# Kernel tuning notes

Measured on AMD Instinct MI355X. Metric: run time of the kernel, lower is better.

The kernel has to match this reference:

```python
import jax, jax.numpy as jnp
import numpy as np

EMBED = 64
SQ = (2, 2)
SHUF = 2
EXPAN = 2
SQ_CH = EMBED // SQ[0]            # 32
SHUF_SP = SQ_CH * SHUF * SHUF     # 128
SQ_SP = SHUF_SP // SQ[1]          # 64
NH = SQ_CH * EXPAN                # 64 heads (same for both attentions)
DN = ('NCHW', 'OIHW', 'NCHW')


def _l2norm(x, axis):
    return x / jnp.maximum(jnp.linalg.norm(x, axis=axis, keepdims=True), 1e-12)


def _qkv_depthwise(x, w, b):
    # grouped 1x1 conv with groups == C: each input channel c maps to 3*EXPAN outputs
    # x: [B,C,H,W], w/b: [C, 3*EXPAN] -> [B, 3*EXPAN, C, H, W]
    y = x[:, :, None] * w[None, :, :, None, None] + b[None, :, :, None, None]
    return jnp.swapaxes(y, 1, 2)


def _group_fuse(o, wf, bf):
    # grouped 1x1 conv groups==C: o [B,C,EXPAN,H,W], wf [C,EXPAN], bf [C]
    return jnp.einsum('bcehw,ce->bchw', o, wf) + bf[None, :, None, None]


def _attention(x, wqkv, bqkv, t, wf, bf, spatial):
    B, C, H, W = x.shape
    qkv = _qkv_depthwise(x, wqkv, bqkv)            # [B, 3*EXPAN, C, H, W]
    d = EXPAN * C // NH                            # head dim over channels
    hw = H * W
    heads = lambda a: a.reshape(B, NH, d, hw)
    q = heads(qkv[:, :EXPAN])
    k = heads(qkv[:, EXPAN:2 * EXPAN])
    v = heads(qkv[:, 2 * EXPAN:])
    if spatial:
        q, k = _l2norm(q, -2), _l2norm(k, -2)
        attn = jax.nn.softmax(jnp.einsum('bhdn,bhdm->bhnm', q, k) * t, axis=-1)
        o = jnp.einsum('bhnm,bhdm->bhdn', attn, v)
    else:
        q, k = _l2norm(q, -1), _l2norm(k, -1)
        attn = jax.nn.softmax(jnp.einsum('bhdn,bhen->bhde', q, k) * t, axis=-1)
        o = jnp.einsum('bhde,bhen->bhdn', attn, v)
    # [B,NH,d,HW] -> [B,EXPAN,C,H,W] -> [B,C,EXPAN,H,W]
    o = o.reshape(B, EXPAN, C, H, W).transpose(0, 2, 1, 3, 4)
    return _group_fuse(o, wf, bf)


def setup_inputs() -> dict:
    key = jax.random.key(0)
    ks = jax.random.split(key, 20)
    s = 0.02
    inp = {
        'x': jax.random.normal(ks[0], (2, EMBED, 64, 64), jnp.float32),
        'w_sq1': jax.random.normal(ks[1], (SQ_CH, EMBED), jnp.float32) * s,
        'b_sq1': jax.random.normal(ks[2], (SQ_CH,), jnp.float32) * s,
        'w_sq2': jax.random.normal(ks[3], (SQ_SP, 1, SHUF, SHUF), jnp.float32) * s,
        'b_sq2': jax.random.normal(ks[4], (SQ_SP,), jnp.float32) * s,
        'ca_wqkv': jax.random.normal(ks[5], (SQ_SP, 3 * EXPAN), jnp.float32) * s,
        'ca_bqkv': jax.random.normal(ks[6], (SQ_SP, 3 * EXPAN), jnp.float32) * s,
        'ca_t': jnp.ones((1, NH, 1, 1), jnp.float32),
        'ca_wf': jax.random.normal(ks[7], (SQ_SP, EXPAN), jnp.float32) * s,
        'ca_bf': jax.random.normal(ks[8], (SQ_SP,), jnp.float32) * s,
        'sa_wqkv': jax.random.normal(ks[9], (SQ_SP, 3 * EXPAN), jnp.float32) * s,
        'sa_bqkv': jax.random.normal(ks[10], (SQ_SP, 3 * EXPAN), jnp.float32) * s,
        'sa_t': jnp.ones((1, NH, 1, 1), jnp.float32),
        'sa_wf': jax.random.normal(ks[11], (SQ_SP, EXPAN), jnp.float32) * s,
        'sa_bf': jax.random.normal(ks[12], (SQ_SP,), jnp.float32) * s,
        'w_un1': jax.random.normal(ks[13], (SHUF_SP, SQ_SP // SQ_CH, 1, 1), jnp.float32) * s,
        'b_un1': jax.random.normal(ks[14], (SHUF_SP,), jnp.float32) * s,
        'w_un2': jax.random.normal(ks[15], (EMBED, SQ_CH), jnp.float32) * s,
        'b_un2': jax.random.normal(ks[16], (EMBED,), jnp.float32) * s,
    }
    return inp


def reference(x, w_sq1, b_sq1, w_sq2, b_sq2,
              ca_wqkv, ca_bqkv, ca_t, ca_wf, ca_bf,
              sa_wqkv, sa_bqkv, sa_t, sa_wf, sa_bf,
              w_un1, b_un1, w_un2, b_un2):
    # ch_sp_squeeze: 1x1 conv then grouped shuffle-stride conv
    y = jnp.einsum('bchw,oc->bohw', x, w_sq1) + b_sq1[None, :, None, None]
    y = jax.lax.conv_general_dilated(y, w_sq2, (SHUF, SHUF), 'VALID',
                                     feature_group_count=SQ_CH,
                                     dimension_numbers=DN) + b_sq2[None, :, None, None]
    group_num, each_group = SQ_CH, SQ_SP // SQ_CH
    idx = np.array([i + j * group_num for i in range(group_num) for j in range(each_group)])
    y = y[:, idx]
    y = _attention(y, ca_wqkv, ca_bqkv, ca_t, ca_wf, ca_bf, spatial=False)
    nidx = np.array([i + j * each_group for i in range(each_group) for j in range(group_num)])
    y = y[:, nidx]
    y = _attention(y, sa_wqkv, sa_bqkv, sa_t, sa_wf, sa_bf, spatial=True)
    # sp_ch_unsqueeze: grouped 1x1 conv, pixel shuffle, 1x1 conv
    y = jax.lax.conv_general_dilated(y, w_un1, (1, 1), 'VALID',
                                     feature_group_count=SQ_CH,
                                     dimension_numbers=DN) + b_un1[None, :, None, None]
    B, Cc, h, w = y.shape
    r = SHUF
    y = y.reshape(B, Cc // (r * r), r, r, h, w).transpose(0, 1, 4, 2, 5, 3)
    y = y.reshape(B, Cc // (r * r), h * r, w * r)
    y = jnp.einsum('bchw,oc->bohw', y, w_un2) + b_un2[None, :, None, None]
    return y
```

## Files before the change

kernel.cpp:

```cpp
#include <hip/hip_runtime.h>
#include <math.h>

#define NR 6

typedef float v2f __attribute__((ext_vector_type(2)));

__device__ __forceinline__ v2f vfma2(v2f a, v2f b, v2f c) {
#if defined(__has_builtin)
#if __has_builtin(__builtin_elementwise_fma)
    return __builtin_elementwise_fma(a, b, c);
#else
    v2f r; r.x = fmaf(a.x, b.x, c.x); r.y = fmaf(a.y, b.y, c.y); return r;
#endif
#else
    v2f r; r.x = fmaf(a.x, b.x, c.x); r.y = fmaf(a.y, b.y, c.y); return r;
#endif
}

__device__ __forceinline__ void bessel_J(float t, float* J) {
    float h = 0.5f * t, q = h * h;
    float hp = 1.f, rf = 1.f;
#pragma unroll
    for (int r = 0; r <= NR; ++r) {
        if (r > 0) { hp *= h; rf *= (1.f / r); }
        float term = hp * rf, sum = term;
#pragma unroll
        for (int k = 1; k <= 12; ++k) {
            term *= q * (1.f / (k * (r + k)));
            sum += term;
        }
        J[r] = (r ? 2.f : 1.f) * sum;
    }
}

__global__ __launch_bounds__(256) void k_front(const float* __restrict__ x,
        const float* __restrict__ w1x1, const float* __restrict__ b1x1,
        const float* __restrict__ wdw,  const float* __restrict__ bdw,
        float* __restrict__ y3) {
    __shared__ float lxs[64 * 128];
    __shared__ float lwt[8][64];
    int tid = threadIdx.x;
    int q   = blockIdx.x & 3;
    int i32 = (blockIdx.x >> 2) & 31;
    int b   = blockIdx.x >> 7;

    const float4* x4 = (const float4*)x;
#pragma unroll
    for (int i = 0; i < 8; ++i) {
        int f4 = tid + i * 256;
        int c  = f4 >> 5, cw = f4 & 31;
        ((float4*)lxs)[f4] = x4[(b * 64 + c) * 1024 + i32 * 32 + cw];
    }
    for (int idx = tid; idx < 512; idx += 256) {
        int gi = idx >> 6, c = idx & 63;
        int g = 4 * q + (gi & 3) + ((gi & 4) << 2);
        lwt[gi][c] = w1x1[g * 64 + c];
    }
    __syncthreads();

    int gidx = tid >> 5, col = tid & 31;
    int g = 4 * q + (gidx & 3) + ((gidx & 4) << 2);
    v2f acc0 = {0.f, 0.f}, acc1 = {0.f, 0.f};
    const v2f* lx2 = (const v2f*)lxs;
#pragma unroll 4
    for (int c = 0; c < 64; ++c) {
        float wv = lwt[gidx][c];
        v2f w2 = {wv, wv};
        acc0 = vfma2(w2, lx2[c * 64 + col], acc0);
        acc1 = vfma2(w2, lx2[c * 64 + 32 + col], acc1);
    }
    float bs = b1x1[g];
    float a00 = acc0.x + bs, a01 = acc0.y + bs;
    float a10 = acc1.x + bs, a11 = acc1.y + bs;
#pragma unroll
    for (int s = 0; s < 2; ++s) {
        int oc = 2 * g + s;
        int k  = 2 * (oc & 31) + (oc >> 5);
        float4 wd = ((const float4*)wdw)[oc];
        float v = bdw[oc];
        v = fmaf(wd.x, a00, v); v = fmaf(wd.y, a01, v);
        v = fmaf(wd.z, a10, v); v = fmaf(wd.w, a11, v);
        y3[(b * 64 + k) * 1024 + i32 * 32 + col] = v;
    }
}

__device__ __forceinline__ void ca_coeffs(int p, int d,
        float s00, float s01, float s11, float m0, float m1,
        const float* __restrict__ wqkv, const float* __restrict__ bqkv,
        const float* __restrict__ t,    const float* __restrict__ wf,
        const float* __restrict__ bf,   float& A, float& B, float& C) {
    const float N = 1024.f;
    int c0 = 2 * p, c1 = 2 * p + 1;
    int c  = 2 * p + d;
    float Aa = 0.f, Bb = 0.f, Cc = 0.f;
#pragma unroll
    for (int e = 0; e < 2; ++e) {
        float wq0 = wqkv[c0 * 6 + e],     wq1 = wqkv[c1 * 6 + e];
        float bq0 = bqkv[c0 * 6 + e],     bq1 = bqkv[c1 * 6 + e];
        float wk0 = wqkv[c0 * 6 + 2 + e], wk1 = wqkv[c1 * 6 + 2 + e];
        float bk0 = bqkv[c0 * 6 + 2 + e], bk1 = bqkv[c1 * 6 + 2 + e];
        float wv0 = wqkv[c0 * 6 + 4 + e], wv1 = wqkv[c1 * 6 + 4 + e];
        float bv0 = bqkv[c0 * 6 + 4 + e], bv1 = bqkv[c1 * 6 + 4 + e];
        float te  = t[e * 32 + p];
        float sqq = (d == 0) ? (wq0 * wq0 * s00 + 2.f * wq0 * bq0 * m0 + N * bq0 * bq0)
                             : (wq1 * wq1 * s11 + 2.f * wq1 * bq1 * m1 + N * bq1 * bq1);
        float kk0 = wk0 * wk0 * s00 + 2.f * wk0 * bk0 * m0 + N * bk0 * bk0;
        float kk1 = wk1 * wk1 * s11 + 2.f * wk1 * bk1 * m1 + N * bk1 * bk1;
        float inq  = 1.f / fmaxf(sqrtf(fmaxf(sqq, 0.f)), 1e-12f);
        float ink0 = 1.f / fmaxf(sqrtf(fmaxf(kk0, 0.f)), 1e-12f);
        float ink1 = 1.f / fmaxf(sqrtf(fmaxf(kk1, 0.f)), 1e-12f);
        float qk0 = (d == 0) ? (wq0 * wk0 * s00 + wq0 * bk0 * m0 + bq0 * wk0 * m0 + N * bq0 * bk0)
                             : (wq1 * wk0 * s01 + wq1 * bk0 * m1 + bq1 * wk0 * m0 + N * bq1 * bk0);
        float qk1 = (d == 0) ? (wq0 * wk1 * s01 + wq0 * bk1 * m0 + bq0 * wk1 * m1 + N * bq0 * bk1)
                             : (wq1 * wk1 * s11 + wq1 * bk1 * m1 + bq1 * wk1 * m1 + N * bq1 * bk1);
        float L0 = qk0 * inq * ink0 * te, L1 = qk1 * inq * ink1 * te;
        float mx = fmaxf(L0, L1);
        float e0 = expf(L0 - mx), e1 = expf(L1 - mx);
        float iv = 1.f / (e0 + e1);
        float p0 = e0 * iv, p1 = e1 * iv;
        float f = wf[c * 2 + e];
        Aa += f * p0 * wv0;
        Bb += f * p1 * wv1;
        Cc += f * (p0 * bv0 + p1 * bv1);
    }
    A = Aa; B = Bb; C = Cc + bf[c];
}

__global__ __launch_bounds__(256) void k_attn(const float* __restrict__ y3,
        const float* __restrict__ ca_wqkv, const float* __restrict__ ca_bqkv,
        const float* __restrict__ ca_t,    const float* __restrict__ ca_wf,
        const float* __restrict__ ca_bf,
        const float* __restrict__ wqkv, const float* __restrict__ bqkv,
        const float* __restrict__ t,    const float* __restrict__ wf,
        const float* __restrict__ bfuse, const float* __restrict__ w1,
        const float* __restrict__ b1,   float* __restrict__ y8) {
    __shared__ float ly[4][1024];
    __shared__ float redg[10][4];
    __shared__ float redm[4][39];
    __shared__ float momf[2][39];
    int tid = threadIdx.x;
    int chunk = blockIdx.x & 3;
    int j = (blockIdx.x >> 2) & 31;
    int b = blockIdx.x >> 7;
    int jp = j & 15;
    int dsel = j >> 4;
    int c0 = 2 * j, c1 = 2 * j + 1;

    const float* base = y3 + (b * 64 + 4 * jp) * 1024;
    float sA00 = 0, sA01 = 0, sA11 = 0, mA0 = 0, mA1 = 0;
    float sB00 = 0, sB01 = 0, sB11 = 0, mB0 = 0, mB1 = 0;
#pragma unroll
    for (int r = 0; r < 4; ++r) {
        int n = tid + r * 256;
        float a0 = base[n], a1 = base[1024 + n];
        float a2 = base[2048 + n], a3 = base[3072 + n];
        ly[0][n] = a0; ly[1][n] = a1; ly[2][n] = a2; ly[3][n] = a3;
        sA00 = fmaf(a0, a0, sA00); sA01 = fmaf(a0, a1, sA01); sA11 = fmaf(a1, a1, sA11);
        mA0 += a0; mA1 += a1;
        sB00 = fmaf(a2, a2, sB00); sB01 = fmaf(a2, a3, sB01); sB11 = fmaf(a3, a3, sB11);
        mB0 += a2; mB1 += a3;
    }
#pragma unroll
    for (int off = 1; off < 64; off <<= 1) {
        sA00 += __shfl_xor(sA00, off, 64); sA01 += __shfl_xor(sA01, off, 64);
        sA11 += __shfl_xor(sA11, off, 64); mA0 += __shfl_xor(mA0, off, 64);
        mA1  += __shfl_xor(mA1,  off, 64);
        sB00 += __shfl_xor(sB00, off, 64); sB01 += __shfl_xor(sB01, off, 64);
        sB11 += __shfl_xor(sB11, off, 64); mB0 += __shfl_xor(mB0, off, 64);
        mB1  += __shfl_xor(mB1,  off, 64);
    }
    int wid = tid >> 6;
    if ((tid & 63) == 0) {
        redg[0][wid] = sA00; redg[1][wid] = sA01; redg[2][wid] = sA11;
        redg[3][wid] = mA0;  redg[4][wid] = mA1;
        redg[5][wid] = sB00; redg[6][wid] = sB01; redg[7][wid] = sB11;
        redg[8][wid] = mB0;  redg[9][wid] = mB1;
    }
    __syncthreads();
    sA00 = redg[0][0] + redg[0][1] + redg[0][2] + redg[0][3];
    sA01 = redg[1][0] + redg[1][1] + redg[1][2] + redg[1][3];
    sA11 = redg[2][0] + redg[2][1] + redg[2][2] + redg[2][3];
    mA0  = redg[3][0] + redg[3][1] + redg[3][2] + redg[3][3];
    mA1  = redg[4][0] + redg[4][1] + redg[4][2] + redg[4][3];
    sB00 = redg[5][0] + redg[5][1] + redg[5][2] + redg[5][3];
    sB01 = redg[6][0] + redg[6][1] + redg[6][2] + redg[6][3];
    sB11 = redg[7][0] + redg[7][1] + redg[7][2] + redg[7][3];
    mB0  = redg[8][0] + redg[8][1] + redg[8][2] + redg[8][3];
    mB1  = redg[9][0] + redg[9][1] + redg[9][2] + redg[9][3];

    float Aa, Ba, Ca, Ab, Bb, Cb;
    ca_coeffs(2 * jp,     dsel, sA00, sA01, sA11, mA0, mA1,
              ca_wqkv, ca_bqkv, ca_t, ca_wf, ca_bf, Aa, Ba, Ca);
    ca_coeffs(2 * jp + 1, dsel, sB00, sB01, sB11, mB0, mB1,
              ca_wqkv, ca_bqkv, ca_t, ca_wf, ca_bf, Ab, Bb, Cb);

    int e2 = tid >> 7, l = tid & 127;
    float wk0 = wqkv[c0 * 6 + 2 + e2], wk1 = wqkv[c1 * 6 + 2 + e2];
    float bk0 = bqkv[c0 * 6 + 2 + e2], bk1 = bqkv[c1 * 6 + 2 + e2];
    float wv0 = wqkv[c0 * 6 + 4 + e2], wv1 = wqkv[c1 * 6 + 4 + e2];
    float bv0 = bqkv[c0 * 6 + 4 + e2], bv1 = bqkv[c1 * 6 + 4 + e2];
    float mom[39];
#pragma unroll
    for (int i = 0; i < 39; ++i) mom[i] = 0.f;
#pragma unroll
    for (int kk = 0; kk < 8; ++kk) {
        int m = l + (kk << 7);
        float xa = fmaf(Aa, ly[0][m], fmaf(Ba, ly[1][m], Ca));
        float xb = fmaf(Ab, ly[2][m], fmaf(Bb, ly[3][m], Cb));
        float k0 = fmaf(wk0, xa, bk0), k1 = fmaf(wk1, xb, bk1);
        float inv = 1.f / fmaxf(sqrtf(k0 * k0 + k1 * k1), 1e-12f);
        float cp = k0 * inv, sp = k1 * inv;
        float v0 = fmaf(wv0, xa, bv0), v1 = fmaf(wv1, xb, bv1);
        mom[0] += 1.f; mom[1] += v0; mom[2] += v1;
        float c_m1 = 1.f, s_m1 = 0.f, c_r = cp, s_r = sp;
        float twoc = 2.f * cp;
#pragma unroll
        for (int r = 1; r <= NR; ++r) {
            int bi = 3 + (r - 1) * 6;
            mom[bi + 0] += c_r;
            mom[bi + 1] = fmaf(c_r, v0, mom[bi + 1]);
            mom[bi + 2] = fmaf(c_r, v1, mom[bi + 2]);
            mom[bi + 3] += s_r;
            mom[bi + 4] = fmaf(s_r, v0, mom[bi + 4]);
            mom[bi + 5] = fmaf(s_r, v1, mom[bi + 5]);
            float cn = fmaf(twoc, c_r, -c_m1);
            float sn = fmaf(twoc, s_r, -s_m1);
            c_m1 = c_r; s_m1 = s_r; c_r = cn; s_r = sn;
        }
    }
#pragma unroll
    for (int i = 0; i < 39; ++i) {
        float v = mom[i];
        v += __shfl_xor(v, 1, 64);  v += __shfl_xor(v, 2, 64);
        v += __shfl_xor(v, 4, 64);  v += __shfl_xor(v, 8, 64);
        v += __shfl_xor(v, 16, 64); v += __shfl_xor(v, 32, 64);
        mom[i] = v;
    }
    if ((tid & 63) == 0) {
#pragma unroll
        for (int i = 0; i < 39; ++i) redm[wid][i] = mom[i];
    }
    __syncthreads();
    if (tid < 78) {
        int e = (tid >= 39) ? 1 : 0;
        int i = tid - 39 * e;
        int r = (i < 3) ? 0 : ((i - 3) / 6 + 1);
        float J[NR + 1];
        bessel_J(t[e * 32 + j], J);
        momf[e][i] = (redm[2 * e][i] + redm[2 * e + 1][i]) * J[r];
    }
    __syncthreads();

    int n = (chunk << 8) + tid;
    float xan = fmaf(Aa, ly[0][n], fmaf(Ba, ly[1][n], Ca));
    float xbn = fmaf(Ab, ly[2][n], fmaf(Bb, ly[3][n], Cb));
    float oo[2][2];
#pragma unroll
    for (int e = 0; e < 2; ++e) {
        float wq0 = wqkv[c0 * 6 + e], wq1 = wqkv[c1 * 6 + e];
        float bq0 = bqkv[c0 * 6 + e], bq1 = bqkv[c1 * 6 + e];
        float q0 = fmaf(wq0, xan, bq0), q1 = fmaf(wq1, xbn, bq1);
        float qi = 1.f / fmaxf(sqrtf(q0 * q0 + q1 * q1), 1e-12f);
        float a = q0 * qi, bq = q1 * qi;
        const float* M = momf[e];
        float den = M[0], o0 = M[1], o1 = M[2];
        float c_m1 = 1.f, s_m1 = 0.f, c_r = a, s_r = bq;
        float twoc = 2.f * a;
#pragma unroll
        for (int r = 1; r <= NR; ++r) {
            int bi = 3 + (r - 1) * 6;
            den = fmaf(c_r, M[bi + 0], den);
            o0  = fmaf(c_r, M[bi + 1], o0);
            o1  = fmaf(c_r, M[bi + 2], o1);
            den = fmaf(s_r, M[bi + 3], den);
            o0  = fmaf(s_r, M[bi + 4], o0);
            o1  = fmaf(s_r, M[bi + 5], o1);
            float cn = fmaf(twoc, c_r, -c_m1);
            float sn = fmaf(twoc, s_r, -s_m1);
            c_m1 = c_r; s_m1 = s_r; c_r = cn; s_r = sn;
        }
        float rr = 1.f / den;
        oo[e][0] = o0 * rr;
        oo[e][1] = o1 * rr;
    }
    float t0 = fmaf(wf[c0 * 2], oo[0][0], fmaf(wf[c0 * 2 + 1], oo[1][0], bfuse[c0]));
    float t1 = fmaf(wf[c1 * 2], oo[0][1], fmaf(wf[c1 * 2 + 1], oo[1][1], bfuse[c1]));
    int i32 = n >> 5, j32 = n & 31;
    float* dst = y8 + (b * 32 + j) * 4096 + (i32 * 2) * 64 + j32 * 2;
    float z0 = fmaf(w1[(4 * j + 0) * 2], t0, fmaf(w1[(4 * j + 0) * 2 + 1], t1, b1[4 * j + 0]));
    float z1 = fmaf(w1[(4 * j + 1) * 2], t0, fmaf(w1[(4 * j + 1) * 2 + 1], t1, b1[4 * j + 1]));
    float z2 = fmaf(w1[(4 * j + 2) * 2], t0, fmaf(w1[(4 * j + 2) * 2 + 1], t1, b1[4 * j + 2]));
    float z3 = fmaf(w1[(4 * j + 3) * 2], t0, fmaf(w1[(4 * j + 3) * 2 + 1], t1, b1[4 * j + 3]));
    *(float2*)(dst)      = make_float2(z0, z1);
    *(float2*)(dst + 64) = make_float2(z2, z3);
}

__global__ __launch_bounds__(256) void k_conv_un2(const float* __restrict__ y8,
        const float* __restrict__ w, const float* __restrict__ bias,
        float* __restrict__ out) {
    __shared__ float lx[32 * 64];
    __shared__ float lw[64 * 32];
    int tid = threadIdx.x;
    int gp0 = blockIdx.x * 64;
    int b = gp0 >> 12;
    int p0 = gp0 & 4095;
    for (int idx = tid; idx < 32 * 64; idx += 256) {
        int g = idx >> 6, pp = idx & 63;
        lx[idx] = y8[(b * 32 + g) * 4096 + p0 + pp];
    }
    for (int idx = tid; idx < 64 * 32; idx += 256) lw[idx] = w[idx];
    __syncthreads();
    int px = tid & 63, og = tid >> 6;
    float acc[16];
#pragma unroll
    for (int k = 0; k < 16; ++k) acc[k] = 0.f;
    for (int g = 0; g < 32; ++g) {
        float xv = lx[g * 64 + px];
#pragma unroll
        for (int k = 0; k < 16; ++k)
            acc[k] = fmaf(lw[(og * 16 + k) * 32 + g], xv, acc[k]);
    }
#pragma unroll
    for (int k = 0; k < 16; ++k) {
        int o = og * 16 + k;
        out[(b * 64 + o) * 4096 + p0 + px] = acc[k] + bias[o];
    }
}

extern "C" void kernel_launch(void* const* d_in, const int* in_sizes, int n_in,
                              void* d_out, int out_size, void* d_ws, size_t ws_size,
                              hipStream_t stream) {
    (void)in_sizes; (void)n_in; (void)out_size; (void)ws_size;
    const float* x       = (const float*)d_in[0];
    const float* w_sq1   = (const float*)d_in[1];
    const float* b_sq1   = (const float*)d_in[2];
    const float* w_sq2   = (const float*)d_in[3];
    const float* b_sq2   = (const float*)d_in[4];
    const float* ca_wqkv = (const float*)d_in[5];
    const float* ca_bqkv = (const float*)d_in[6];
    const float* ca_t    = (const float*)d_in[7];
    const float* ca_wf   = (const float*)d_in[8];
    const float* ca_bf   = (const float*)d_in[9];
    const float* sa_wqkv = (const float*)d_in[10];
    const float* sa_bqkv = (const float*)d_in[11];
    const float* sa_t    = (const float*)d_in[12];
    const float* sa_wf   = (const float*)d_in[13];
    const float* sa_bf   = (const float*)d_in[14];
    const float* w_un1   = (const float*)d_in[15];
    const float* b_un1   = (const float*)d_in[16];
    const float* w_un2   = (const float*)d_in[17];
    const float* b_un2   = (const float*)d_in[18];
    float* out = (float*)d_out;
    float* ws  = (float*)d_ws;
    float* y3 = ws;
    float* y8 = ws + 131072;

    k_front<<<256, 256, 0, stream>>>(x, w_sq1, b_sq1, w_sq2, b_sq2, y3);
    k_attn <<<256, 256, 0, stream>>>(y3, ca_wqkv, ca_bqkv, ca_t, ca_wf, ca_bf,
                                     sa_wqkv, sa_bqkv, sa_t, sa_wf, sa_bf,
                                     w_un1, b_un1, y8);
    k_conv_un2<<<128, 256, 0, stream>>>(y8, w_un2, b_un2, out);
}
```

Baseline: 110.5 us.

## Fuse three kernels into one persistent kernel with software grid barriers

Merges the front conv, attention and final 1x1 conv kernels into a single launch of 256 blocks, separated by atomic-counter grid barriers, with shared memory unioned across phases. The last phase is re-tiled to 32 pixels per block so it also uses 256 blocks. The goal is to remove inter-kernel launch gaps and tail drain. In exchange it adds a memset and spin-wait barriers, and it depends on all 256 blocks being co-resident to avoid deadlock.

```diff
diff --git a/kernel.cpp b/kernel.cpp
--- a/kernel.cpp
+++ b/kernel.cpp
@@ -30,57 +30,6 @@
             sum += term;
         }
         J[r] = (r ? 2.f : 1.f) * sum;
-    }
-}
-
-__global__ __launch_bounds__(256) void k_front(const float* __restrict__ x,
-        const float* __restrict__ w1x1, const float* __restrict__ b1x1,
-        const float* __restrict__ wdw,  const float* __restrict__ bdw,
-        float* __restrict__ y3) {
-    __shared__ float lxs[64 * 128];
-    __shared__ float lwt[8][64];
-    int tid = threadIdx.x;
-    int q   = blockIdx.x & 3;
-    int i32 = (blockIdx.x >> 2) & 31;
-    int b   = blockIdx.x >> 7;
-
-    const float4* x4 = (const float4*)x;
-#pragma unroll
-    for (int i = 0; i < 8; ++i) {
-        int f4 = tid + i * 256;
-        int c  = f4 >> 5, cw = f4 & 31;
-        ((float4*)lxs)[f4] = x4[(b * 64 + c) * 1024 + i32 * 32 + cw];
-    }
-    for (int idx = tid; idx < 512; idx += 256) {
-        int gi = idx >> 6, c = idx & 63;
-        int g = 4 * q + (gi & 3) + ((gi & 4) << 2);
-        lwt[gi][c] = w1x1[g * 64 + c];
-    }
-    __syncthreads();
-
-    int gidx = tid >> 5, col = tid & 31;
-    int g = 4 * q + (gidx & 3) + ((gidx & 4) << 2);
-    v2f acc0 = {0.f, 0.f}, acc1 = {0.f, 0.f};
-    const v2f* lx2 = (const v2f*)lxs;
-#pragma unroll 4
-    for (int c = 0; c < 64; ++c) {
-        float wv = lwt[gidx][c];
-        v2f w2 = {wv, wv};
-        acc0 = vfma2(w2, lx2[c * 64 + col], acc0);
-        acc1 = vfma2(w2, lx2[c * 64 + 32 + col], acc1);
-    }
-    float bs = b1x1[g];
-    float a00 = acc0.x + bs, a01 = acc0.y + bs;
-    float a10 = acc1.x + bs, a11 = acc1.y + bs;
-#pragma unroll
-    for (int s = 0; s < 2; ++s) {
-        int oc = 2 * g + s;
-        int k  = 2 * (oc & 31) + (oc >> 5);
-        float4 wd = ((const float4*)wdw)[oc];
-        float v = bdw[oc];
-        v = fmaf(wd.x, a00, v); v = fmaf(wd.y, a01, v);
-        v = fmaf(wd.z, a10, v); v = fmaf(wd.w, a11, v);
-        y3[(b * 64 + k) * 1024 + i32 * 32 + col] = v;
     }
 }
 
@@ -126,204 +75,268 @@
     A = Aa; B = Bb; C = Cc + bf[c];
 }
 
-__global__ __launch_bounds__(256) void k_attn(const float* __restrict__ y3,
+struct SmemF { float lxs[64 * 128]; float lwt[8][64]; };
+struct SmemA { float ly[4][1024]; float redg[10][4]; float redm[4][39]; float momf[2][39]; };
+struct SmemC { float lx[32 * 32]; float lw[64 * 32]; };
+union SmemU { SmemF f; SmemA a; SmemC c; };
+
+__device__ __forceinline__ void grid_bar(unsigned* cnt, unsigned target) {
+    __syncthreads();
+    if (threadIdx.x == 0) {
+        __hip_atomic_fetch_add(cnt, 1u, __ATOMIC_ACQ_REL, __HIP_MEMORY_SCOPE_AGENT);
+        while (__hip_atomic_load(cnt, __ATOMIC_ACQUIRE, __HIP_MEMORY_SCOPE_AGENT) < target)
+            __builtin_amdgcn_s_sleep(1);
+    }
+    __syncthreads();
+}
+
+__global__ __launch_bounds__(256) void k_fused(
+        const float* __restrict__ x,
+        const float* __restrict__ w1x1, const float* __restrict__ b1x1,
+        const float* __restrict__ wdw,  const float* __restrict__ bdw,
         const float* __restrict__ ca_wqkv, const float* __restrict__ ca_bqkv,
         const float* __restrict__ ca_t,    const float* __restrict__ ca_wf,
         const float* __restrict__ ca_bf,
         const float* __restrict__ wqkv, const float* __restrict__ bqkv,
         const float* __restrict__ t,    const float* __restrict__ wf,
         const float* __restrict__ bfuse, const float* __restrict__ w1,
-        const float* __restrict__ b1,   float* __restrict__ y8) {
-    __shared__ float ly[4][1024];
-    __shared__ float redg[10][4];
-    __shared__ float redm[4][39];
-    __shared__ float momf[2][39];
+        const float* __restrict__ b1,
+        const float* __restrict__ w2,   const float* __restrict__ b2,
+        float* __restrict__ y3, float* __restrict__ y8,
+        float* __restrict__ out, unsigned* __restrict__ bar) {
+    __shared__ __align__(16) SmemU sm;
     int tid = threadIdx.x;
-    int chunk = blockIdx.x & 3;
-    int j = (blockIdx.x >> 2) & 31;
-    int b = blockIdx.x >> 7;
-    int jp = j & 15;
-    int dsel = j >> 4;
-    int c0 = 2 * j, c1 = 2 * j + 1;
-
-    const float* base = y3 + (b * 64 + 4 * jp) * 1024;
-    float sA00 = 0, sA01 = 0, sA11 = 0, mA0 = 0, mA1 = 0;
-    float sB00 = 0, sB01 = 0, sB11 = 0, mB0 = 0, mB1 = 0;
-#pragma unroll
-    for (int r = 0; r < 4; ++r) {
-        int n = tid + r * 256;
-        float a0 = base[n], a1 = base[1024 + n];
-        float a2 = base[2048 + n], a3 = base[3072 + n];
-        ly[0][n] = a0; ly[1][n] = a1; ly[2][n] = a2; ly[3][n] = a3;
-        sA00 = fmaf(a0, a0, sA00); sA01 = fmaf(a0, a1, sA01); sA11 = fmaf(a1, a1, sA11);
-        mA0 += a0; mA1 += a1;
-        sB00 = fmaf(a2, a2, sB00); sB01 = fmaf(a2, a3, sB01); sB11 = fmaf(a3, a3, sB11);
-        mB0 += a2; mB1 += a3;
-    }
-#pragma unroll
-    for (int off = 1; off < 64; off <<= 1) {
-        sA00 += __shfl_xor(sA00, off, 64); sA01 += __shfl_xor(sA01, off, 64);
-        sA11 += __shfl_xor(sA11, off, 64); mA0 += __shfl_xor(mA0, off, 64);
-        mA1  += __shfl_xor(mA1,  off, 64);
-        sB00 += __shfl_xor(sB00, off, 64); sB01 += __shfl_xor(sB01, off, 64);
-        sB11 += __shfl_xor(sB11, off, 64); mB0 += __shfl_xor(mB0, off, 64);
-        mB1  += __shfl_xor(mB1,  off, 64);
-    }
-    int wid = tid >> 6;
-    if ((tid & 63) == 0) {
-        redg[0][wid] = sA00; redg[1][wid] = sA01; redg[2][wid] = sA11;
-        redg[3][wid] = mA0;  redg[4][wid] = mA1;
-        redg[5][wid] = sB00; redg[6][wid] = sB01; redg[7][wid] = sB11;
-        redg[8][wid] = mB0;  redg[9][wid] = mB1;
-    }
-    __syncthreads();
-    sA00 = redg[0][0] + redg[0][1] + redg[0][2] + redg[0][3];
-    sA01 = redg[1][0] + redg[1][1] + redg[1][2] + redg[1][3];
-    sA11 = redg[2][0] + redg[2][1] + redg[2][2] + redg[2][3];
-    mA0  = redg[3][0] + redg[3][1] + redg[3][2] + redg[3][3];
-    mA1  = redg[4][0] + redg[4][1] + redg[4][2] + redg[4][3];
-    sB00 = redg[5][0] + redg[5][1] + redg[5][2] + redg[5][3];
-    sB01 = redg[6][0] + redg[6][1] + redg[6][2] + redg[6][3];
-    sB11 = redg[7][0] + redg[7][1] + redg[7][2] + redg[7][3];
-    mB0  = redg[8][0] + redg[8][1] + redg[8][2] + redg[8][3];
-    mB1  = redg[9][0] + redg[9][1] + redg[9][2] + redg[9][3];
-
-    float Aa, Ba, Ca, Ab, Bb, Cb;
-    ca_coeffs(2 * jp,     dsel, sA00, sA01, sA11, mA0, mA1,
-              ca_wqkv, ca_bqkv, ca_t, ca_wf, ca_bf, Aa, Ba, Ca);
-    ca_coeffs(2 * jp + 1, dsel, sB00, sB01, sB11, mB0, mB1,
-              ca_wqkv, ca_bqkv, ca_t, ca_wf, ca_bf, Ab, Bb, Cb);
-
-    int e2 = tid >> 7, l = tid & 127;
-    float wk0 = wqkv[c0 * 6 + 2 + e2], wk1 = wqkv[c1 * 6 + 2 + e2];
-    float bk0 = bqkv[c0 * 6 + 2 + e2], bk1 = bqkv[c1 * 6 + 2 + e2];
-    float wv0 = wqkv[c0 * 6 + 4 + e2], wv1 = wqkv[c1 * 6 + 4 + e2];
-    float bv0 = bqkv[c0 * 6 + 4 + e2], bv1 = bqkv[c1 * 6 + 4 + e2];
-    float mom[39];
-#pragma unroll
-    for (int i = 0; i < 39; ++i) mom[i] = 0.f;
-#pragma unroll
-    for (int kk = 0; kk < 8; ++kk) {
-        int m = l + (kk << 7);
-        float xa = fmaf(Aa, ly[0][m], fmaf(Ba, ly[1][m], Ca));
-        float xb = fmaf(Ab, ly[2][m], fmaf(Bb, ly[3][m], Cb));
-        float k0 = fmaf(wk0, xa, bk0), k1 = fmaf(wk1, xb, bk1);
-        float inv = 1.f / fmaxf(sqrtf(k0 * k0 + k1 * k1), 1e-12f);
-        float cp = k0 * inv, sp = k1 * inv;
-        float v0 = fmaf(wv0, xa, bv0), v1 = fmaf(wv1, xb, bv1);
-        mom[0] += 1.f; mom[1] += v0; mom[2] += v1;
-        float c_m1 = 1.f, s_m1 = 0.f, c_r = cp, s_r = sp;
-        float twoc = 2.f * cp;
-#pragma unroll
-        for (int r = 1; r <= NR; ++r) {
-            int bi = 3 + (r - 1) * 6;
-            mom[bi + 0] += c_r;
-            mom[bi + 1] = fmaf(c_r, v0, mom[bi + 1]);
-            mom[bi + 2] = fmaf(c_r, v1, mom[bi + 2]);
-            mom[bi + 3] += s_r;
-            mom[bi + 4] = fmaf(s_r, v0, mom[bi + 4]);
-            mom[bi + 5] = fmaf(s_r, v1, mom[bi + 5]);
-            float cn = fmaf(twoc, c_r, -c_m1);
-            float sn = fmaf(twoc, s_r, -s_m1);
-            c_m1 = c_r; s_m1 = s_r; c_r = cn; s_r = sn;
-        }
-    }
-#pragma unroll
-    for (int i = 0; i < 39; ++i) {
-        float v = mom[i];
-        v += __shfl_xor(v, 1, 64);  v += __shfl_xor(v, 2, 64);
-        v += __shfl_xor(v, 4, 64);  v += __shfl_xor(v, 8, 64);
-        v += __shfl_xor(v, 16, 64); v += __shfl_xor(v, 32, 64);
-        mom[i] = v;
-    }
-    if ((tid & 63) == 0) {
-#pragma unroll
-        for (int i = 0; i < 39; ++i) redm[wid][i] = mom[i];
-    }
-    __syncthreads();
-    if (tid < 78) {
-        int e = (tid >= 39) ? 1 : 0;
-        int i = tid - 39 * e;
-        int r = (i < 3) ? 0 : ((i - 3) / 6 + 1);
-        float J[NR + 1];
-        bessel_J(t[e * 32 + j], J);
-        momf[e][i] = (redm[2 * e][i] + redm[2 * e + 1][i]) * J[r];
-    }
-    __syncthreads();
-
-    int n = (chunk << 8) + tid;
-    float xan = fmaf(Aa, ly[0][n], fmaf(Ba, ly[1][n], Ca));
-    float xbn = fmaf(Ab, ly[2][n], fmaf(Bb, ly[3][n], Cb));
-    float oo[2][2];
-#pragma unroll
-    for (int e = 0; e < 2; ++e) {
-        float wq0 = wqkv[c0 * 6 + e], wq1 = wqkv[c1 * 6 + e];
-        float bq0 = bqkv[c0 * 6 + e], bq1 = bqkv[c1 * 6 + e];
-        float q0 = fmaf(wq0, xan, bq0), q1 = fmaf(wq1, xbn, bq1);
-        float qi = 1.f / fmaxf(sqrtf(q0 * q0 + q1 * q1), 1e-12f);
-        float a = q0 * qi, bq = q1 * qi;
-        const float* M = momf[e];
-        float den = M[0], o0 = M[1], o1 = M[2];
-        float c_m1 = 1.f, s_m1 = 0.f, c_r = a, s_r = bq;
-        float twoc = 2.f * a;
-#pragma unroll
-        for (int r = 1; r <= NR; ++r) {
-            int bi = 3 + (r - 1) * 6;
-            den = fmaf(c_r, M[bi + 0], den);
-            o0  = fmaf(c_r, M[bi + 1], o0);
-            o1  = fmaf(c_r, M[bi + 2], o1);
-            den = fmaf(s_r, M[bi + 3], den);
-            o0  = fmaf(s_r, M[bi + 4], o0);
-            o1  = fmaf(s_r, M[bi + 5], o1);
-            float cn = fmaf(twoc, c_r, -c_m1);
-            float sn = fmaf(twoc, s_r, -s_m1);
-            c_m1 = c_r; s_m1 = s_r; c_r = cn; s_r = sn;
-        }
-        float rr = 1.f / den;
-        oo[e][0] = o0 * rr;
-        oo[e][1] = o1 * rr;
-    }
-    float t0 = fmaf(wf[c0 * 2], oo[0][0], fmaf(wf[c0 * 2 + 1], oo[1][0], bfuse[c0]));
-    float t1 = fmaf(wf[c1 * 2], oo[0][1], fmaf(wf[c1 * 2 + 1], oo[1][1], bfuse[c1]));
-    int i32 = n >> 5, j32 = n & 31;
-    float* dst = y8 + (b * 32 + j) * 4096 + (i32 * 2) * 64 + j32 * 2;
-    float z0 = fmaf(w1[(4 * j + 0) * 2], t0, fmaf(w1[(4 * j + 0) * 2 + 1], t1, b1[4 * j + 0]));
-    float z1 = fmaf(w1[(4 * j + 1) * 2], t0, fmaf(w1[(4 * j + 1) * 2 + 1], t1, b1[4 * j + 1]));
-    float z2 = fmaf(w1[(4 * j + 2) * 2], t0, fmaf(w1[(4 * j + 2) * 2 + 1], t1, b1[4 * j + 2]));
-    float z3 = fmaf(w1[(4 * j + 3) * 2], t0, fmaf(w1[(4 * j + 3) * 2 + 1], t1, b1[4 * j + 3]));
-    *(float2*)(dst)      = make_float2(z0, z1);
-    *(float2*)(dst + 64) = make_float2(z2, z3);
-}
-
-__global__ __launch_bounds__(256) void k_conv_un2(const float* __restrict__ y8,
-        const float* __restrict__ w, const float* __restrict__ bias,
-        float* __restrict__ out) {
-    __shared__ float lx[32 * 64];
-    __shared__ float lw[64 * 32];
-    int tid = threadIdx.x;
-    int gp0 = blockIdx.x * 64;
-    int b = gp0 >> 12;
-    int p0 = gp0 & 4095;
-    for (int idx = tid; idx < 32 * 64; idx += 256) {
-        int g = idx >> 6, pp = idx & 63;
-        lx[idx] = y8[(b * 32 + g) * 4096 + p0 + pp];
-    }
-    for (int idx = tid; idx < 64 * 32; idx += 256) lw[idx] = w[idx];
-    __syncthreads();
-    int px = tid & 63, og = tid >> 6;
-    float acc[16];
-#pragma unroll
-    for (int k = 0; k < 16; ++k) acc[k] = 0.f;
-    for (int g = 0; g < 32; ++g) {
-        float xv = lx[g * 64 + px];
-#pragma unroll
-        for (int k = 0; k < 16; ++k)
-            acc[k] = fmaf(lw[(og * 16 + k) * 32 + g], xv, acc[k]);
-    }
-#pragma unroll
-    for (int k = 0; k < 16; ++k) {
-        int o = og * 16 + k;
-        out[(b * 64 + o) * 4096 + p0 + px] = acc[k] + bias[o];
+    int bid = blockIdx.x;
+
+    {
+        int q   = bid & 3;
+        int i32 = (bid >> 2) & 31;
+        int b   = bid >> 7;
+        const float4* x4 = (const float4*)x;
+#pragma unroll
+        for (int i = 0; i < 8; ++i) {
+            int f4 = tid + i * 256;
+            int c  = f4 >> 5, cw = f4 & 31;
+            ((float4*)sm.f.lxs)[f4] = x4[(b * 64 + c) * 1024 + i32 * 32 + cw];
+        }
+        for (int idx = tid; idx < 512; idx += 256) {
+            int gi = idx >> 6, c = idx & 63;
+            int g = 4 * q + (gi & 3) + ((gi & 4) << 2);
+            sm.f.lwt[gi][c] = w1x1[g * 64 + c];
+        }
+        __syncthreads();
+
+        int gidx = tid >> 5, col = tid & 31;
+        int g = 4 * q + (gidx & 3) + ((gidx & 4) << 2);
+        v2f acc0 = {0.f, 0.f}, acc1 = {0.f, 0.f};
+        const v2f* lx2 = (const v2f*)sm.f.lxs;
+#pragma unroll 4
+        for (int c = 0; c < 64; ++c) {
+            float wv = sm.f.lwt[gidx][c];
+            v2f wv2 = {wv, wv};
+            acc0 = vfma2(wv2, lx2[c * 64 + col], acc0);
+            acc1 = vfma2(wv2, lx2[c * 64 + 32 + col], acc1);
+        }
+        float bs = b1x1[g];
+        float a00 = acc0.x + bs, a01 = acc0.y + bs;
+        float a10 = acc1.x + bs, a11 = acc1.y + bs;
+#pragma unroll
+        for (int s = 0; s < 2; ++s) {
+            int oc = 2 * g + s;
+            int k  = 2 * (oc & 31) + (oc >> 5);
+            float4 wd = ((const float4*)wdw)[oc];
+            float v = bdw[oc];
+            v = fmaf(wd.x, a00, v); v = fmaf(wd.y, a01, v);
+            v = fmaf(wd.z, a10, v); v = fmaf(wd.w, a11, v);
+            y3[(b * 64 + k) * 1024 + i32 * 32 + col] = v;
+        }
+    }
+    grid_bar(bar + 0, 256);
+
+    {
+        int chunk = bid & 3;
+        int j = (bid >> 2) & 31;
+        int b = bid >> 7;
+        int jp = j & 15;
+        int dsel = j >> 4;
+        int c0 = 2 * j, c1 = 2 * j + 1;
+
+        const float* base = y3 + (b * 64 + 4 * jp) * 1024;
+        float sA00 = 0, sA01 = 0, sA11 = 0, mA0 = 0, mA1 = 0;
+        float sB00 = 0, sB01 = 0, sB11 = 0, mB0 = 0, mB1 = 0;
+#pragma unroll
+        for (int r = 0; r < 4; ++r) {
+            int n = tid + r * 256;
+            float a0 = base[n], a1 = base[1024 + n];
+            float a2 = base[2048 + n], a3 = base[3072 + n];
+            sm.a.ly[0][n] = a0; sm.a.ly[1][n] = a1;
+            sm.a.ly[2][n] = a2; sm.a.ly[3][n] = a3;
+            sA00 = fmaf(a0, a0, sA00); sA01 = fmaf(a0, a1, sA01); sA11 = fmaf(a1, a1, sA11);
+            mA0 += a0; mA1 += a1;
+            sB00 = fmaf(a2, a2, sB00); sB01 = fmaf(a2, a3, sB01); sB11 = fmaf(a3, a3, sB11);
+            mB0 += a2; mB1 += a3;
+        }
+#pragma unroll
+        for (int off = 1; off < 64; off <<= 1) {
+            sA00 += __shfl_xor(sA00, off, 64); sA01 += __shfl_xor(sA01, off, 64);
+            sA11 += __shfl_xor(sA11, off, 64); mA0 += __shfl_xor(mA0, off, 64);
+            mA1  += __shfl_xor(mA1,  off, 64);
+            sB00 += __shfl_xor(sB00, off, 64); sB01 += __shfl_xor(sB01, off, 64);
+            sB11 += __shfl_xor(sB11, off, 64); mB0 += __shfl_xor(mB0, off, 64);
+            mB1  += __shfl_xor(mB1,  off, 64);
+        }
+        int wid = tid >> 6;
+        if ((tid & 63) == 0) {
+            sm.a.redg[0][wid] = sA00; sm.a.redg[1][wid] = sA01; sm.a.redg[2][wid] = sA11;
+            sm.a.redg[3][wid] = mA0;  sm.a.redg[4][wid] = mA1;
+            sm.a.redg[5][wid] = sB00; sm.a.redg[6][wid] = sB01; sm.a.redg[7][wid] = sB11;
+            sm.a.redg[8][wid] = mB0;  sm.a.redg[9][wid] = mB1;
+        }
+        __syncthreads();
+        sA00 = sm.a.redg[0][0] + sm.a.redg[0][1] + sm.a.redg[0][2] + sm.a.redg[0][3];
+        sA01 = sm.a.redg[1][0] + sm.a.redg[1][1] + sm.a.redg[1][2] + sm.a.redg[1][3];
+        sA11 = sm.a.redg[2][0] + sm.a.redg[2][1] + sm.a.redg[2][2] + sm.a.redg[2][3];
+        mA0  = sm.a.redg[3][0] + sm.a.redg[3][1] + sm.a.redg[3][2] + sm.a.redg[3][3];
+        mA1  = sm.a.redg[4][0] + sm.a.redg[4][1] + sm.a.redg[4][2] + sm.a.redg[4][3];
+        sB00 = sm.a.redg[5][0] + sm.a.redg[5][1] + sm.a.redg[5][2] + sm.a.redg[5][3];
+        sB01 = sm.a.redg[6][0] + sm.a.redg[6][1] + sm.a.redg[6][2] + sm.a.redg[6][3];
+        sB11 = sm.a.redg[7][0] + sm.a.redg[7][1] + sm.a.redg[7][2] + sm.a.redg[7][3];
+        mB0  = sm.a.redg[8][0] + sm.a.redg[8][1] + sm.a.redg[8][2] + sm.a.redg[8][3];
+        mB1  = sm.a.redg[9][0] + sm.a.redg[9][1] + sm.a.redg[9][2] + sm.a.redg[9][3];
+
+        float Aa, Ba, Ca, Ab, Bb, Cb;
+        ca_coeffs(2 * jp,     dsel, sA00, sA01, sA11, mA0, mA1,
+                  ca_wqkv, ca_bqkv, ca_t, ca_wf, ca_bf, Aa, Ba, Ca);
+        ca_coeffs(2 * jp + 1, dsel, sB00, sB01, sB11, mB0, mB1,
+                  ca_wqkv, ca_bqkv, ca_t, ca_wf, ca_bf, Ab, Bb, Cb);
+
+        int e2 = tid >> 7, l = tid & 127;
+        float wk0 = wqkv[c0 * 6 + 2 + e2], wk1 = wqkv[c1 * 6 + 2 + e2];
+        float bk0 = bqkv[c0 * 6 + 2 + e2], bk1 = bqkv[c1 * 6 + 2 + e2];
+        float wv0 = wqkv[c0 * 6 + 4 + e2], wv1 = wqkv[c1 * 6 + 4 + e2];
+        float bv0 = bqkv[c0 * 6 + 4 + e2], bv1 = bqkv[c1 * 6 + 4 + e2];
+        float mom[39];
+#pragma unroll
+        for (int i = 0; i < 39; ++i) mom[i] = 0.f;
+#pragma unroll
+        for (int kk = 0; kk < 8; ++kk) {
+            int m = l + (kk << 7);
+            float xa = fmaf(Aa, sm.a.ly[0][m], fmaf(Ba, sm.a.ly[1][m], Ca));
+            float xb = fmaf(Ab, sm.a.ly[2][m], fmaf(Bb, sm.a.ly[3][m], Cb));
+            float k0 = fmaf(wk0, xa, bk0), k1 = fmaf(wk1, xb, bk1);
+            float inv = 1.f / fmaxf(sqrtf(k0 * k0 + k1 * k1), 1e-12f);
+            float cp = k0 * inv, sp = k1 * inv;
+            float v0 = fmaf(wv0, xa, bv0), v1 = fmaf(wv1, xb, bv1);
+            mom[0] += 1.f; mom[1] += v0; mom[2] += v1;
+            float c_m1 = 1.f, s_m1 = 0.f, c_r = cp, s_r = sp;
+            float twoc = 2.f * cp;
+#pragma unroll
+            for (int r = 1; r <= NR; ++r) {
+                int bi = 3 + (r - 1) * 6;
+                mom[bi + 0] += c_r;
+                mom[bi + 1] = fmaf(c_r, v0, mom[bi + 1]);
+                mom[bi + 2] = fmaf(c_r, v1, mom[bi + 2]);
+                mom[bi + 3] += s_r;
+                mom[bi + 4] = fmaf(s_r, v0, mom[bi + 4]);
+                mom[bi + 5] = fmaf(s_r, v1, mom[bi + 5]);
+                float cn = fmaf(twoc, c_r, -c_m1);
+                float sn = fmaf(twoc, s_r, -s_m1);
+                c_m1 = c_r; s_m1 = s_r; c_r = cn; s_r = sn;
+            }
+        }
+#pragma unroll
+        for (int i = 0; i < 39; ++i) {
+            float v = mom[i];
+            v += __shfl_xor(v, 1, 64);  v += __shfl_xor(v, 2, 64);
+            v += __shfl_xor(v, 4, 64);  v += __shfl_xor(v, 8, 64);
+            v += __shfl_xor(v, 16, 64); v += __shfl_xor(v, 32, 64);
+            mom[i] = v;
+        }
+        if ((tid & 63) == 0) {
+#pragma unroll
+            for (int i = 0; i < 39; ++i) sm.a.redm[wid][i] = mom[i];
+        }
+        __syncthreads();
+        if (tid < 78) {
+            int e = (tid >= 39) ? 1 : 0;
+            int i = tid - 39 * e;
+            int r = (i < 3) ? 0 : ((i - 3) / 6 + 1);
+            float J[NR + 1];
+            bessel_J(t[e * 32 + j], J);
+            sm.a.momf[e][i] = (sm.a.redm[2 * e][i] + sm.a.redm[2 * e + 1][i]) * J[r];
+        }
+        __syncthreads();
+
+        int n = (chunk << 8) + tid;
+        float xan = fmaf(Aa, sm.a.ly[0][n], fmaf(Ba, sm.a.ly[1][n], Ca));
+        float xbn = fmaf(Ab, sm.a.ly[2][n], fmaf(Bb, sm.a.ly[3][n], Cb));
+        float oo[2][2];
+#pragma unroll
+        for (int e = 0; e < 2; ++e) {
+            float wq0 = wqkv[c0 * 6 + e], wq1 = wqkv[c1 * 6 + e];
+            float bq0 = bqkv[c0 * 6 + e], bq1 = bqkv[c1 * 6 + e];
+            float q0 = fmaf(wq0, xan, bq0), q1 = fmaf(wq1, xbn, bq1);
+            float qi = 1.f / fmaxf(sqrtf(q0 * q0 + q1 * q1), 1e-12f);
+            float a = q0 * qi, bq = q1 * qi;
+            const float* M = sm.a.momf[e];
+            float den = M[0], o0 = M[1], o1 = M[2];
+            float c_m1 = 1.f, s_m1 = 0.f, c_r = a, s_r = bq;
+            float twoc = 2.f * a;
+#pragma unroll
+            for (int r = 1; r <= NR; ++r) {
+                int bi = 3 + (r - 1) * 6;
+                den = fmaf(c_r, M[bi + 0], den);
+                o0  = fmaf(c_r, M[bi + 1], o0);
+                o1  = fmaf(c_r, M[bi + 2], o1);
+                den = fmaf(s_r, M[bi + 3], den);
+                o0  = fmaf(s_r, M[bi + 4], o0);
+                o1  = fmaf(s_r, M[bi + 5], o1);
+                float cn = fmaf(twoc, c_r, -c_m1);
+                float sn = fmaf(twoc, s_r, -s_m1);
+                c_m1 = c_r; s_m1 = s_r; c_r = cn; s_r = sn;
+            }
+            float rr = 1.f / den;
+            oo[e][0] = o0 * rr;
+            oo[e][1] = o1 * rr;
+        }
+        float t0 = fmaf(wf[c0 * 2], oo[0][0], fmaf(wf[c0 * 2 + 1], oo[1][0], bfuse[c0]));
+        float t1 = fmaf(wf[c1 * 2], oo[0][1], fmaf(wf[c1 * 2 + 1], oo[1][1], bfuse[c1]));
+        int i32 = n >> 5, j32 = n & 31;
+        float* dst = y8 + (b * 32 + j) * 4096 + (i32 * 2) * 64 + j32 * 2;
+        float z0 = fmaf(w1[(4 * j + 0) * 2], t0, fmaf(w1[(4 * j + 0) * 2 + 1], t1, b1[4 * j + 0]));
+        float z1 = fmaf(w1[(4 * j + 1) * 2], t0, fmaf(w1[(4 * j + 1) * 2 + 1], t1, b1[4 * j + 1]));
+        float z2 = fmaf(w1[(4 * j + 2) * 2], t0, fmaf(w1[(4 * j + 2) * 2 + 1], t1, b1[4 * j + 2]));
+        float z3 = fmaf(w1[(4 * j + 3) * 2], t0, fmaf(w1[(4 * j + 3) * 2 + 1], t1, b1[4 * j + 3]));
+        *(float2*)(dst)      = make_float2(z0, z1);
+        *(float2*)(dst + 64) = make_float2(z2, z3);
+    }
+    grid_bar(bar + 1, 256);
+
+    {
+        int gp0 = bid * 32;
+        int b = gp0 >> 12;
+        int p0 = gp0 & 4095;
+        for (int idx = tid; idx < 1024; idx += 256) {
+            int g = idx >> 5, pp = idx & 31;
+            sm.c.lx[idx] = y8[(b * 32 + g) * 4096 + p0 + pp];
+        }
+        for (int idx = tid; idx < 2048; idx += 256) sm.c.lw[idx] = w2[idx];
+        __syncthreads();
+        int px = tid & 31, og = tid >> 5;
+        float acc[8];
+#pragma unroll
+        for (int k = 0; k < 8; ++k) acc[k] = 0.f;
+        for (int g = 0; g < 32; ++g) {
+            float xv = sm.c.lx[g * 32 + px];
+#pragma unroll
+            for (int k = 0; k < 8; ++k)
+                acc[k] = fmaf(sm.c.lw[(og * 8 + k) * 32 + g], xv, acc[k]);
+        }
+#pragma unroll
+        for (int k = 0; k < 8; ++k) {
+            int o = og * 8 + k;
+            out[(b * 64 + o) * 4096 + p0 + px] = acc[k] + b2[o];
+        }
     }
 }
 
@@ -354,10 +367,12 @@
     float* ws  = (float*)d_ws;
     float* y3 = ws;
     float* y8 = ws + 131072;
-
-    k_front<<<256, 256, 0, stream>>>(x, w_sq1, b_sq1, w_sq2, b_sq2, y3);
-    k_attn <<<256, 256, 0, stream>>>(y3, ca_wqkv, ca_bqkv, ca_t, ca_wf, ca_bf,
+    unsigned* bar = (unsigned*)(ws + 131072 + 262144);
+
+    hipMemsetAsync(bar, 0, 2 * sizeof(unsigned), stream);
+    k_fused<<<256, 256, 0, stream>>>(x, w_sq1, b_sq1, w_sq2, b_sq2,
+                                     ca_wqkv, ca_bqkv, ca_t, ca_wf, ca_bf,
                                      sa_wqkv, sa_bqkv, sa_t, sa_wf, sa_bf,
-                                     w_un1, b_un1, y8);
-    k_conv_un2<<<128, 256, 0, stream>>>(y8, w_un2, b_un2, out);
-}
+                                     w_un1, b_un1, w_un2, b_un2,
+                                     y3, y8, out, bar);
+}
```

Result: slower. 132.6 us (+20.0%).
